# Kernel optimization log

Measured on AMD Instinct MI355X. Metric: run time of the kernel, lower is better.

Reference implementation:

```python
import jax, jax.numpy as jnp
import numpy as np

B, T, H, O = 256, 2048, 64, 2


def setup_inputs() -> dict:
    key = jax.random.key(0)
    ks = jax.random.split(key, 14)
    def lin(k, out_f, in_f):
        bound = np.sqrt(6.0 / (in_f + out_f))
        return jax.random.uniform(k, (out_f, in_f), jnp.float32, -bound, bound)
    return {
        "x": jax.random.normal(ks[0], (B, T, 2), jnp.float32),
        "h0": jax.random.normal(ks[1], (1, B, H), jnp.float32),
        "Wa": lin(ks[2], H, H + 1), "ba": jnp.zeros((H,), jnp.float32),
        "Wp1": lin(ks[3], H, H + 1), "bp1": jnp.zeros((H,), jnp.float32),
        "Wp2": lin(ks[4], H, H + 1), "bp2": jnp.zeros((H,), jnp.float32),
        "Wf": lin(ks[5], H, 2 * H), "bf": jnp.zeros((H,), jnp.float32),
        "Wg": lin(ks[6], H, 2 * H), "bg": jnp.zeros((H,), jnp.float32),
        "Wo": lin(ks[7], O, H), "bo": jnp.zeros((O,), jnp.float32),
    }


def reference(x, h0, Wa, ba, Wp1, bp1, Wp2, bp2, Wf, bf, Wg, bg, Wo, bo):
    # x: [B, T, 2] (I/Q), h0: [1, B, H]
    xt = jnp.swapaxes(x, 0, 1)  # [T, B, 2]

    def step(h, x_t):
        i = x_t[:, 0:1]
        q = x_t[:, 1:2]
        amp = jnp.sqrt(i * i + q * q)
        theta = jnp.arctan2(q, i)
        cos_t = jnp.cos(theta)
        sin_t = jnp.sin(theta)
        a = jnp.tanh(jnp.concatenate([h, amp], -1) @ Wa.T + ba)
        p1 = jnp.tanh(jnp.concatenate([h, cos_t], -1) @ Wp1.T + bp1)
        p2 = jnp.tanh(jnp.concatenate([h, sin_t], -1) @ Wp2.T + bp2)
        u = a * p1 * p2 * (1 - a) * (1 - p1) * (1 - p2)
        hu = jnp.concatenate([h, u], -1)
        f = jax.nn.sigmoid(hu @ Wf.T + bf)
        g = jnp.tanh(hu @ Wg.T + bg)
        h_new = f * h + (1 - f) * g
        y = h_new @ Wo.T + bo
        return h_new, y

    _, ys = jax.lax.scan(step, h0[0], xt)  # ys: [T, B, O]
    return jnp.swapaxes(ys, 0, 1)  # [B, T, O]
```

## Files before the change

### kernel.cpp

```cpp
#include <hip/hip_runtime.h>
#include <math.h>

#define BB 256
#define TT 2048
#define HH 64

typedef _Float16 half2v __attribute__((ext_vector_type(2)));
typedef __fp16  fp16v2 __attribute__((ext_vector_type(2)));
union H2I { half2v h; int i; };

__device__ __forceinline__ float tanh_fast(float v) {
    float e = __expf(2.0f * v);
    return 1.0f - 2.0f / (e + 1.0f);
}

__device__ __forceinline__ float fdot2(half2v a, half2v b, float c) {
    return __builtin_amdgcn_fdot2(a, b, c, false);
}

__device__ __forceinline__ half2v pack_pair(float a, float b) {
    fp16v2 r = __builtin_amdgcn_cvt_pkrtz(a, b);
    return __builtin_bit_cast(half2v, r);
}

__device__ __forceinline__ void pin_h2(half2v& v) {
    H2I u; u.h = v;
    asm volatile("" : "+v"(u.i));
    v = u.h;
}

__device__ __forceinline__ half2v bcast_pair(half2v v, int lane) {
    H2I u; u.h = v;
    H2I w; w.i = __builtin_amdgcn_readlane(u.i, lane);
    return w.h;
}

__device__ __forceinline__ float dpp_neighbor(float v) {
    return __int_as_float(__builtin_amdgcn_mov_dpp(__float_as_int(v), 0xB1, 0xf, 0xf, true));
}

template <int CTRL>
__device__ __forceinline__ float dpp_add_stage(float v) {
    int t = __builtin_amdgcn_update_dpp(0, __float_as_int(v), CTRL, 0xf, 0xf, true);
    return v + __int_as_float(t);
}

__device__ __forceinline__ float wave_sum_dpp(float v) {
    v = dpp_add_stage<0x111>(v);
    v = dpp_add_stage<0x112>(v);
    v = dpp_add_stage<0x114>(v);
    v = dpp_add_stage<0x118>(v);
    v = dpp_add_stage<0x142>(v);
    v = dpp_add_stage<0x143>(v);
    return v;
}

__global__ __launch_bounds__(256, 1)
void pgjanet_kernel(const float* __restrict__ x,
                    const float* __restrict__ h0,
                    const float* __restrict__ Wa,  const float* __restrict__ ba,
                    const float* __restrict__ Wp1, const float* __restrict__ bp1,
                    const float* __restrict__ Wp2, const float* __restrict__ bp2,
                    const float* __restrict__ Wf,  const float* __restrict__ bf,
                    const float* __restrict__ Wg,  const float* __restrict__ bg,
                    const float* __restrict__ Wo,  const float* __restrict__ bo,
                    float* __restrict__ out)
{
    const int b   = blockIdx.x;
    const int tid = threadIdx.x;
    const int j   = tid & 63;
    const int w   = __builtin_amdgcn_readfirstlane(tid >> 6);
    const int kb  = w * 16;

    __shared__ float xs[TT * 2];
    __shared__ float ybuf[TT * 2];
    __shared__ float partA[3][4][HH];
    __shared__ float partC[2][4][HH];

    {
        const float* xp = x + (size_t)b * (TT * 2);
        for (int i = tid; i < TT * 2; i += 256) xs[i] = xp[i];
    }

    half2v wa[8], wp1[8], wp2[8], wfh[8], wfu[8], wgh[8], wgu[8];
#pragma unroll
    for (int m = 0; m < 8; ++m) {
        const int k = kb + 2 * m;
        wa[m]  = pack_pair(Wa [j * (HH + 1) + k], Wa [j * (HH + 1) + k + 1]);
        wp1[m] = pack_pair(Wp1[j * (HH + 1) + k], Wp1[j * (HH + 1) + k + 1]);
        wp2[m] = pack_pair(Wp2[j * (HH + 1) + k], Wp2[j * (HH + 1) + k + 1]);
        wfh[m] = pack_pair(Wf [j * (2 * HH) + k], Wf [j * (2 * HH) + k + 1]);
        wfu[m] = pack_pair(Wf [j * (2 * HH) + HH + k], Wf [j * (2 * HH) + HH + k + 1]);
        wgh[m] = pack_pair(Wg [j * (2 * HH) + k], Wg [j * (2 * HH) + k + 1]);
        wgu[m] = pack_pair(Wg [j * (2 * HH) + HH + k], Wg [j * (2 * HH) + HH + k + 1]);
    }
#pragma unroll
    for (int m = 0; m < 8; ++m) {
        pin_h2(wa[m]);  pin_h2(wp1[m]); pin_h2(wp2[m]);
        pin_h2(wfh[m]); pin_h2(wfu[m]); pin_h2(wgh[m]); pin_h2(wgu[m]);
    }

    const float waH  = Wa [j * (HH + 1) + HH];
    const float wp1H = Wp1[j * (HH + 1) + HH];
    const float wp2H = Wp2[j * (HH + 1) + HH];
    const float ba_r = ba[j], bp1_r = bp1[j], bp2_r = bp2[j];
    const float bf_r = bf[j], bg_r = bg[j];
    const float wo0 = Wo[j], wo1 = Wo[HH + j];
    const float bo0 = bo[0], bo1 = bo[1];

    float h = h0[b * HH + j];
    float* yp = out + (size_t)b * (TT * 2);

    __syncthreads();
    float xi = xs[0], xq = xs[1];

    for (int t = 0; t < TT; ++t) {
        const int tn = (t + 1 < TT) ? (t + 1) : (TT - 1);
        float xi_n = xs[2 * tn];
        float xq_n = xs[2 * tn + 1];

        float hnbr = dpp_neighbor(h);
        half2v hp = pack_pair(h, hnbr);
        half2v sh[8];
#pragma unroll
        for (int m = 0; m < 8; ++m) sh[m] = bcast_pair(hp, kb + 2 * m);

        float va = 0.f, v1 = 0.f, v2 = 0.f, vf = 0.f, vg = 0.f;
#pragma unroll
        for (int m = 0; m < 8; ++m) {
            va = fdot2(sh[m], wa[m],  va);
            v1 = fdot2(sh[m], wp1[m], v1);
            v2 = fdot2(sh[m], wp2[m], v2);
            vf = fdot2(sh[m], wfh[m], vf);
            vg = fdot2(sh[m], wgh[m], vg);
        }
        partA[0][w][j] = va;
        partA[1][w][j] = v1;
        partA[2][w][j] = v2;

        float amp = sqrtf(xi * xi + xq * xq);
        float inv = (amp > 0.f) ? (1.0f / amp) : 0.0f;
        float ct  = (amp > 0.f) ? (xi * inv) : 1.0f;
        float st  = xq * inv;

        __syncthreads();

        float pre_a = (partA[0][0][j] + partA[0][1][j]) + (partA[0][2][j] + partA[0][3][j])
                    + fmaf(amp, waH, ba_r);
        float pre_1 = (partA[1][0][j] + partA[1][1][j]) + (partA[1][2][j] + partA[1][3][j])
                    + fmaf(ct, wp1H, bp1_r);
        float pre_2 = (partA[2][0][j] + partA[2][1][j]) + (partA[2][2][j] + partA[2][3][j])
                    + fmaf(st, wp2H, bp2_r);
        float a  = tanh_fast(pre_a);
        float p1 = tanh_fast(pre_1);
        float p2 = tanh_fast(pre_2);
        float u  = (a * (1.f - a)) * (p1 * (1.f - p1)) * (p2 * (1.f - p2));

        float unbr = dpp_neighbor(u);
        half2v up = pack_pair(u, unbr);
        half2v su[8];
#pragma unroll
        for (int m = 0; m < 8; ++m) su[m] = bcast_pair(up, kb + 2 * m);

        float uf = vf, ug = vg;
#pragma unroll
        for (int m = 0; m < 8; ++m) {
            uf = fdot2(su[m], wfu[m], uf);
            ug = fdot2(su[m], wgu[m], ug);
        }
        partC[0][w][j] = uf;
        partC[1][w][j] = ug;

        __syncthreads();

        float pre_f = (partC[0][0][j] + partC[0][1][j]) + (partC[0][2][j] + partC[0][3][j]) + bf_r;
        float pre_g = (partC[1][0][j] + partC[1][1][j]) + (partC[1][2][j] + partC[1][3][j]) + bg_r;
        float f = 1.0f / (1.0f + __expf(-pre_f));
        float g = tanh_fast(pre_g);
        h = fmaf(f, h - g, g);

        if (w == (t & 3)) {
            float y0 = wave_sum_dpp(h * wo0);
            float y1 = wave_sum_dpp(h * wo1);
            if (j == 63) {
                ybuf[2 * t]     = y0 + bo0;
                ybuf[2 * t + 1] = y1 + bo1;
            }
        }

        xi = xi_n; xq = xq_n;
    }

    __syncthreads();
    {
        const float4* ys4 = reinterpret_cast<const float4*>(ybuf);
        float4*       yp4 = reinterpret_cast<float4*>(yp);
#pragma unroll
        for (int i = tid; i < TT * 2 / 4; i += 256) yp4[i] = ys4[i];
    }
}

extern "C" void kernel_launch(void* const* d_in, const int* in_sizes, int n_in,
                              void* d_out, int out_size, void* d_ws, size_t ws_size,
                              hipStream_t stream) {
    const float* x   = (const float*)d_in[0];
    const float* h0  = (const float*)d_in[1];
    const float* Wa  = (const float*)d_in[2];
    const float* ba  = (const float*)d_in[3];
    const float* Wp1 = (const float*)d_in[4];
    const float* bp1 = (const float*)d_in[5];
    const float* Wp2 = (const float*)d_in[6];
    const float* bp2 = (const float*)d_in[7];
    const float* Wf  = (const float*)d_in[8];
    const float* bf  = (const float*)d_in[9];
    const float* Wg  = (const float*)d_in[10];
    const float* bg  = (const float*)d_in[11];
    const float* Wo  = (const float*)d_in[12];
    const float* bo  = (const float*)d_in[13];
    float* out = (float*)d_out;

    pgjanet_kernel<<<dim3(BB), dim3(256), 0, stream>>>(
        x, h0, Wa, ba, Wp1, bp1, Wp2, bp2, Wf, bf, Wg, bg, Wo, bo, out);
}
```

Before: 1.634 ms.

## Split gates across waves and compute u-path redundantly to drop one barrier per step

Instead of splitting the K dimension of every gate across the four waves, each wave now owns whole gates: waves 0-2 compute a, p1, p2 with full 64-wide dot products, and wave 3 computes the h-parts of f and g. After one barrier, every wave redundantly computes u and the full u-contribution to f and g, so the second barrier per step goes away. The exchange buffer is double-buffered by step parity. Fast rcp/rsq intrinsics replace divisions and sqrt. The cost is more registers (128 packed weight pairs per lane), a 4x redundant u-dot product, and a load imbalance on wave 3.

```diff
diff --git a/kernel.cpp b/kernel.cpp
--- a/kernel.cpp
+++ b/kernel.cpp
@@ -9,9 +9,24 @@
 typedef __fp16  fp16v2 __attribute__((ext_vector_type(2)));
 union H2I { half2v h; int i; };
 
+#if __has_builtin(__builtin_amdgcn_rcpf)
+__device__ __forceinline__ float fast_rcp(float v) { return __builtin_amdgcn_rcpf(v); }
+#else
+__device__ __forceinline__ float fast_rcp(float v) { return 1.0f / v; }
+#endif
+#if __has_builtin(__builtin_amdgcn_rsqf)
+__device__ __forceinline__ float fast_rsq(float v) { return __builtin_amdgcn_rsqf(v); }
+#else
+__device__ __forceinline__ float fast_rsq(float v) { return rsqrtf(v); }
+#endif
+
 __device__ __forceinline__ float tanh_fast(float v) {
     float e = __expf(2.0f * v);
-    return 1.0f - 2.0f / (e + 1.0f);
+    return fmaf(-2.0f, fast_rcp(e + 1.0f), 1.0f);
+}
+
+__device__ __forceinline__ float sigmoid_fast(float v) {
+    return fast_rcp(1.0f + __expf(-v));
 }
 
 __device__ __forceinline__ float fdot2(half2v a, half2v b, float c) {
@@ -70,40 +85,38 @@
     const int tid = threadIdx.x;
     const int j   = tid & 63;
     const int w   = __builtin_amdgcn_readfirstlane(tid >> 6);
-    const int kb  = w * 16;
 
     __shared__ float xs[TT * 2];
     __shared__ float ybuf[TT * 2];
-    __shared__ float partA[3][4][HH];
-    __shared__ float partC[2][4][HH];
+    __shared__ float exch[2][5][HH];
 
     {
         const float* xp = x + (size_t)b * (TT * 2);
         for (int i = tid; i < TT * 2; i += 256) xs[i] = xp[i];
     }
 
-    half2v wa[8], wp1[8], wp2[8], wfh[8], wfu[8], wgh[8], wgu[8];
-#pragma unroll
-    for (int m = 0; m < 8; ++m) {
-        const int k = kb + 2 * m;
-        wa[m]  = pack_pair(Wa [j * (HH + 1) + k], Wa [j * (HH + 1) + k + 1]);
-        wp1[m] = pack_pair(Wp1[j * (HH + 1) + k], Wp1[j * (HH + 1) + k + 1]);
-        wp2[m] = pack_pair(Wp2[j * (HH + 1) + k], Wp2[j * (HH + 1) + k + 1]);
-        wfh[m] = pack_pair(Wf [j * (2 * HH) + k], Wf [j * (2 * HH) + k + 1]);
-        wfu[m] = pack_pair(Wf [j * (2 * HH) + HH + k], Wf [j * (2 * HH) + HH + k + 1]);
-        wgh[m] = pack_pair(Wg [j * (2 * HH) + k], Wg [j * (2 * HH) + k + 1]);
-        wgu[m] = pack_pair(Wg [j * (2 * HH) + HH + k], Wg [j * (2 * HH) + HH + k + 1]);
-    }
-#pragma unroll
-    for (int m = 0; m < 8; ++m) {
-        pin_h2(wa[m]);  pin_h2(wp1[m]); pin_h2(wp2[m]);
-        pin_h2(wfh[m]); pin_h2(wfu[m]); pin_h2(wgh[m]); pin_h2(wgu[m]);
-    }
-
-    const float waH  = Wa [j * (HH + 1) + HH];
-    const float wp1H = Wp1[j * (HH + 1) + HH];
-    const float wp2H = Wp2[j * (HH + 1) + HH];
-    const float ba_r = ba[j], bp1_r = bp1[j], bp2_r = bp2[j];
+    const float* gsrc  = (w == 0) ? Wa : (w == 1) ? Wp1 : (w == 2) ? Wp2 : Wf;
+    const int    gld   = (w < 3) ? (HH + 1) : (2 * HH);
+    const float* g2src = (w == 3) ? Wg : gsrc;
+    const int    g2ld  = (w == 3) ? (2 * HH) : gld;
+
+    half2v wgate[32], wgate2[32], wfuv[32], wguv[32];
+#pragma unroll
+    for (int m = 0; m < 32; ++m) {
+        wgate[m]  = pack_pair(gsrc [j * gld  + 2 * m], gsrc [j * gld  + 2 * m + 1]);
+        wgate2[m] = pack_pair(g2src[j * g2ld + 2 * m], g2src[j * g2ld + 2 * m + 1]);
+        wfuv[m]   = pack_pair(Wf[j * (2 * HH) + HH + 2 * m], Wf[j * (2 * HH) + HH + 2 * m + 1]);
+        wguv[m]   = pack_pair(Wg[j * (2 * HH) + HH + 2 * m], Wg[j * (2 * HH) + HH + 2 * m + 1]);
+    }
+#pragma unroll
+    for (int m = 0; m < 32; ++m) {
+        pin_h2(wgate[m]); pin_h2(wgate2[m]); pin_h2(wfuv[m]); pin_h2(wguv[m]);
+    }
+
+    const float xw   = (w == 0) ? Wa [j * (HH + 1) + HH]
+                     : (w == 1) ? Wp1[j * (HH + 1) + HH]
+                     : (w == 2) ? Wp2[j * (HH + 1) + HH] : 0.f;
+    const float bsel = (w == 0) ? ba[j] : (w == 1) ? bp1[j] : (w == 2) ? bp2[j] : 0.f;
     const float bf_r = bf[j], bg_r = bg[j];
     const float wo0 = Wo[j], wo1 = Wo[HH + j];
     const float bo0 = bo[0], bo1 = bo[1];
@@ -112,71 +125,96 @@
     float* yp = out + (size_t)b * (TT * 2);
 
     __syncthreads();
-    float xi = xs[0], xq = xs[1];
+
+    float xsel;
+    {
+        float xi = xs[0], xq = xs[1];
+        float r2 = xi * xi + xq * xq;
+        float rsq = fast_rsq(r2);
+        bool ok = r2 > 0.f;
+        float amp = ok ? r2 * rsq : 0.f;
+        float ct  = ok ? xi * rsq : 1.f;
+        float st  = ok ? xq * rsq : 0.f;
+        xsel = (w == 0) ? amp : (w == 1) ? ct : st;
+    }
 
     for (int t = 0; t < TT; ++t) {
+        float (*ex)[HH] = exch[t & 1];
+
         const int tn = (t + 1 < TT) ? (t + 1) : (TT - 1);
-        float xi_n = xs[2 * tn];
-        float xq_n = xs[2 * tn + 1];
+        float xi_n = xs[2 * tn], xq_n = xs[2 * tn + 1];
+        float xsel_n;
+        {
+            float r2 = xi_n * xi_n + xq_n * xq_n;
+            float rsq = fast_rsq(r2);
+            bool ok = r2 > 0.f;
+            float amp = ok ? r2 * rsq : 0.f;
+            float ct  = ok ? xi_n * rsq : 1.f;
+            float st  = ok ? xq_n * rsq : 0.f;
+            xsel_n = (w == 0) ? amp : (w == 1) ? ct : st;
+        }
 
         float hnbr = dpp_neighbor(h);
         half2v hp = pack_pair(h, hnbr);
-        half2v sh[8];
-#pragma unroll
-        for (int m = 0; m < 8; ++m) sh[m] = bcast_pair(hp, kb + 2 * m);
-
-        float va = 0.f, v1 = 0.f, v2 = 0.f, vf = 0.f, vg = 0.f;
+        half2v sh[32];
+#pragma unroll
+        for (int m = 0; m < 32; ++m) sh[m] = bcast_pair(hp, 2 * m);
+
+        float a0 = 0.f, a1 = 0.f, a2 = 0.f, a3 = 0.f;
 #pragma unroll
         for (int m = 0; m < 8; ++m) {
-            va = fdot2(sh[m], wa[m],  va);
-            v1 = fdot2(sh[m], wp1[m], v1);
-            v2 = fdot2(sh[m], wp2[m], v2);
-            vf = fdot2(sh[m], wfh[m], vf);
-            vg = fdot2(sh[m], wgh[m], vg);
-        }
-        partA[0][w][j] = va;
-        partA[1][w][j] = v1;
-        partA[2][w][j] = v2;
-
-        float amp = sqrtf(xi * xi + xq * xq);
-        float inv = (amp > 0.f) ? (1.0f / amp) : 0.0f;
-        float ct  = (amp > 0.f) ? (xi * inv) : 1.0f;
-        float st  = xq * inv;
+            a0 = fdot2(sh[m],      wgate[m],      a0);
+            a1 = fdot2(sh[m + 8],  wgate[m + 8],  a1);
+            a2 = fdot2(sh[m + 16], wgate[m + 16], a2);
+            a3 = fdot2(sh[m + 24], wgate[m + 24], a3);
+        }
+        float pre = (a0 + a1) + (a2 + a3);
+
+        if (w == 3) {
+            float b0 = 0.f, b1 = 0.f, b2 = 0.f, b3 = 0.f;
+#pragma unroll
+            for (int m = 0; m < 8; ++m) {
+                b0 = fdot2(sh[m],      wgate2[m],      b0);
+                b1 = fdot2(sh[m + 8],  wgate2[m + 8],  b1);
+                b2 = fdot2(sh[m + 16], wgate2[m + 16], b2);
+                b3 = fdot2(sh[m + 24], wgate2[m + 24], b3);
+            }
+            ex[3][j] = pre + bf_r;
+            ex[4][j] = ((b0 + b1) + (b2 + b3)) + bg_r;
+        } else {
+            ex[w][j] = tanh_fast(pre + fmaf(xsel, xw, bsel));
+        }
 
         __syncthreads();
 
-        float pre_a = (partA[0][0][j] + partA[0][1][j]) + (partA[0][2][j] + partA[0][3][j])
-                    + fmaf(amp, waH, ba_r);
-        float pre_1 = (partA[1][0][j] + partA[1][1][j]) + (partA[1][2][j] + partA[1][3][j])
-                    + fmaf(ct, wp1H, bp1_r);
-        float pre_2 = (partA[2][0][j] + partA[2][1][j]) + (partA[2][2][j] + partA[2][3][j])
-                    + fmaf(st, wp2H, bp2_r);
-        float a  = tanh_fast(pre_a);
-        float p1 = tanh_fast(pre_1);
-        float p2 = tanh_fast(pre_2);
-        float u  = (a * (1.f - a)) * (p1 * (1.f - p1)) * (p2 * (1.f - p2));
+        float av  = ex[0][j];
+        float pv1 = ex[1][j];
+        float pv2 = ex[2][j];
+        float fh  = ex[3][j];
+        float gh  = ex[4][j];
+        float u = (av * (1.f - av)) * (pv1 * (1.f - pv1)) * (pv2 * (1.f - pv2));
 
         float unbr = dpp_neighbor(u);
-        half2v up = pack_pair(u, unbr);
-        half2v su[8];
-#pragma unroll
-        for (int m = 0; m < 8; ++m) su[m] = bcast_pair(up, kb + 2 * m);
-
-        float uf = vf, ug = vg;
+        half2v upk = pack_pair(u, unbr);
+        half2v su[32];
+#pragma unroll
+        for (int m = 0; m < 32; ++m) su[m] = bcast_pair(upk, 2 * m);
+
+        float f0 = 0.f, f1 = 0.f, f2 = 0.f, f3 = 0.f;
+        float g0 = 0.f, g1 = 0.f, g2 = 0.f, g3 = 0.f;
 #pragma unroll
         for (int m = 0; m < 8; ++m) {
-            uf = fdot2(su[m], wfu[m], uf);
-            ug = fdot2(su[m], wgu[m], ug);
-        }
-        partC[0][w][j] = uf;
-        partC[1][w][j] = ug;
-
-        __syncthreads();
-
-        float pre_f = (partC[0][0][j] + partC[0][1][j]) + (partC[0][2][j] + partC[0][3][j]) + bf_r;
-        float pre_g = (partC[1][0][j] + partC[1][1][j]) + (partC[1][2][j] + partC[1][3][j]) + bg_r;
-        float f = 1.0f / (1.0f + __expf(-pre_f));
-        float g = tanh_fast(pre_g);
+            f0 = fdot2(su[m],      wfuv[m],      f0);
+            f1 = fdot2(su[m + 8],  wfuv[m + 8],  f1);
+            f2 = fdot2(su[m + 16], wfuv[m + 16], f2);
+            f3 = fdot2(su[m + 24], wfuv[m + 24], f3);
+            g0 = fdot2(su[m],      wguv[m],      g0);
+            g1 = fdot2(su[m + 8],  wguv[m + 8],  g1);
+            g2 = fdot2(su[m + 16], wguv[m + 16], g2);
+            g3 = fdot2(su[m + 24], wguv[m + 24], g3);
+        }
+        float f = sigmoid_fast(fh + (f0 + f1) + (f2 + f3));
+        float g = tanh_fast(gh + (g0 + g1) + (g2 + g3));
         h = fmaf(f, h - g, g);
 
         if (w == (t & 3)) {
@@ -188,14 +226,13 @@
             }
         }
 
-        xi = xi_n; xq = xq_n;
+        xsel = xsel_n;
     }
 
     __syncthreads();
     {
         const float4* ys4 = reinterpret_cast<const float4*>(ybuf);
         float4*       yp4 = reinterpret_cast<float4*>(yp);
-#pragma unroll
         for (int i = tid; i < TT * 2 / 4; i += 256) yp4[i] = ys4[i];
     }
 }
```

Result: faster. 1.512 ms (-7.4%).
